# Optimization experiments

Hardware: AMD Instinct MI355X
Metric: run time of the kernel (lower is better)

Reference implementation:

```python
import jax, jax.numpy as jnp
import numpy as np

K = 64                      # sort-pool k
B_GRAPHS, N_PER = 256, 512  # graphs, nodes per graph
DIM_F, E_PER = 128, 8192    # node feature dim, edges per graph
EMB = 32


def setup_inputs() -> dict:
    key = jax.random.key(0)
    ks = jax.random.split(key, 12)
    N = B_GRAPHS * N_PER
    off = (jnp.arange(B_GRAPHS) * N_PER)[:, None]
    x = jax.random.normal(ks[0], (N, DIM_F), jnp.float32)
    edge_src = (jax.random.randint(ks[1], (B_GRAPHS, E_PER), 0, N_PER) + off).reshape(-1)
    edge_dst = (jax.random.randint(ks[2], (B_GRAPHS, E_PER), 0, N_PER) + off).reshape(-1)

    def lin(k, o, i):
        return (jax.random.normal(k, (o, i), jnp.float32) / np.float32(np.sqrt(i)))

    return {
        "x": x,
        "W0": lin(ks[3], EMB, DIM_F), "b0": jnp.zeros((EMB,), jnp.float32),
        "W1": lin(ks[4], EMB, EMB),   "b1": jnp.zeros((EMB,), jnp.float32),
        "W2": lin(ks[5], EMB, EMB),   "b2": jnp.zeros((EMB,), jnp.float32),
        "W3": lin(ks[6], 1, EMB),     "b3": jnp.zeros((1,), jnp.float32),
        "conv1_w": jax.random.normal(ks[7], (16, 1, 97), jnp.float32) / np.float32(np.sqrt(97.0)),
        "conv1_b": jnp.zeros((16,), jnp.float32),
        "conv2_w": jax.random.normal(ks[8], (32, 16, 5), jnp.float32) / np.float32(np.sqrt(80.0)),
        "conv2_b": jnp.zeros((32,), jnp.float32),
        "d1_w": lin(ks[9], 128, 896),  "d1_b": jnp.zeros((128,), jnp.float32),
        "d2_w": lin(ks[10], 10, 128),  "d2_b": jnp.zeros((10,), jnp.float32),
        "edge_src": edge_src, "edge_dst": edge_dst,
        "num_graphs": B_GRAPHS,
    }


def _dgcnn_conv(h_in, W, b, src, dst):
    # h = lin(x); message = (1/deg_src)[dst] * h[src]; scatter-add at dst
    N = h_in.shape[0]
    h = h_in @ W.T + b
    deg = jax.ops.segment_sum(jnp.ones_like(src, dtype=h.dtype), src, num_segments=N)
    norm = 1.0 / deg                       # self-loops guarantee deg >= 1
    msg = h[src] * norm[dst][:, None]      # [E+N, C]
    return jax.ops.segment_sum(msg, dst, num_segments=N)


def _forward(x, W0, b0, W1, b1, W2, b2, W3, b3,
             conv1_w, conv1_b, conv2_w, conv2_b,
             d1_w, d1_b, d2_w, d2_b, src, dst, num_graphs):
    N = x.shape[0]
    self_idx = jnp.arange(N)
    src = jnp.concatenate([src, self_idx])   # add_self_loops
    dst = jnp.concatenate([dst, self_idx])
    hs = []
    h = x
    for (W, b) in ((W0, b0), (W1, b1), (W2, b2), (W3, b3)):
        h = jnp.tanh(_dgcnn_conv(h, W, b, src, dst))
        hs.append(h)
    feat = jnp.concatenate(hs, axis=1)       # [N, 97]
    D = feat.shape[1]
    B = num_graphs
    n = N // B
    g = feat.reshape(B, n, D)
    # global_sort_pool: sort nodes per graph by last channel, descending, take top-k
    order = jnp.argsort(-g[:, :, -1], axis=1)[:, :K]
    topk = jnp.take_along_axis(g, order[:, :, None], axis=1)   # [B, K, D]
    # Conv1d(1,16,kernel=D,stride=D) over [B,1,K*D] == per-node linear on D
    c1 = jax.nn.relu(jnp.einsum('bkd,od->bok', topk, conv1_w[:, 0, :])
                     + conv1_b[None, :, None])                  # [B,16,K]
    p = c1.reshape(B, 16, K // 2, 2).max(axis=-1)               # MaxPool1d(2,2)
    c2 = jax.lax.conv_general_dilated(p, conv2_w, (1,), 'VALID',
                                      dimension_numbers=('NCH', 'OIH', 'NCH'))
    c2 = jax.nn.relu(c2 + conv2_b[None, :, None])               # [B,32,28]
    flat = c2.reshape(B, -1)                                    # [B,896]
    hid = jax.nn.relu(flat @ d1_w.T + d1_b)                     # dropout = identity (eval)
    return hid @ d2_w.T + d2_b                                  # [B,10]


def reference(x, W0, b0, W1, b1, W2, b2, W3, b3,
              conv1_w, conv1_b, conv2_w, conv2_b,
              d1_w, d1_b, d2_w, d2_b, edge_src, edge_dst, num_graphs):
    return _forward(x, W0, b0, W1, b1, W2, b2, W3, b3,
                    conv1_w, conv1_b, conv2_w, conv2_b,
                    d1_w, d1_b, d2_w, d2_b, edge_src, edge_dst, num_graphs)
```

## Files before the change

### kernel.cpp

```cpp
#include <hip/hip_runtime.h>

#define NG   256
#define NP   512
#define EPG  8192
#define FDIM 128
#define STB  36

#define OFF_STAGE 0
#define OFF_BUFB  65536
#define OFF_CSR   139264
#define OFF_OFFS  155648
#define OFF_WT    156680
#define OFF_CUR   156712
#define OFF_DCNT  158760
#define OFF_NRM   160808
#define SMEM_SZ   162856

#define OFF_KEY  OFF_CSR
#define OFF_IDX  (OFF_CSR + 2048)
#define OFF_L3   OFF_CUR
#define FO_FEAT 0
#define FO_C1   6208
#define FO_P    7232
#define FO_C2   7744
#define FO_HID  8640

__global__ __launch_bounds__(1024, 4) void dgcnn_fused(
    const float* __restrict__ x,
    const float* __restrict__ W0, const float* __restrict__ b0,
    const float* __restrict__ W1, const float* __restrict__ b1,
    const float* __restrict__ W2, const float* __restrict__ b2,
    const float* __restrict__ W3, const float* __restrict__ b3,
    const float* __restrict__ c1w, const float* __restrict__ c1b,
    const float* __restrict__ c2w, const float* __restrict__ c2b,
    const float* __restrict__ d1w, const float* __restrict__ d1b,
    const float* __restrict__ d2w, const float* __restrict__ d2b,
    const int* __restrict__ esrc, const int* __restrict__ edst,
    float* __restrict__ hs1, float* __restrict__ hs2,
    float* __restrict__ out)
{
  extern __shared__ char smem[];
  float*          stageF = (float*)(smem + OFF_STAGE);
  float*          bufB  = (float*)(smem + OFF_BUFB);
  unsigned short* csr   = (unsigned short*)(smem + OFF_CSR);
  unsigned short* offs  = (unsigned short*)(smem + OFF_OFFS);
  unsigned int*   wt    = (unsigned int*)(smem + OFF_WT);
  unsigned int*   cur   = (unsigned int*)(smem + OFF_CUR);
  unsigned int*   dcnt  = (unsigned int*)(smem + OFF_DCNT);
  float*          nrm   = (float*)(smem + OFF_NRM);
  float*          lin3S = (float*)(smem + OFF_L3);
  float*          keyA  = (float*)(smem + OFF_KEY);
  unsigned int*   idxA  = (unsigned int*)(smem + OFF_IDX);

  const int g    = blockIdx.x;
  const int tid  = threadIdx.x;
  const int lane = tid & 63;
  const int wv   = __builtin_amdgcn_readfirstlane(tid >> 6);
  const int half = __builtin_amdgcn_readfirstlane(tid >> 9);
  const int v    = tid & 511;
  const int nb   = g * NP;
  const size_t gb = (size_t)g * (NP * 32);

  const int ldRow0 = tid >> 3;
  const int ldGrp  = tid & 7;
  const int ldSwz  = (ldGrp ^ (ldRow0 & 7)) * 16;
  auto load_chunk = [&](int kc, float4* xr) {
    const float* base = x + (size_t)nb * FDIM + kc * 32 + ldGrp * 4;
#pragma unroll
    for (int it = 0; it < 4; it++)
      xr[it] = *(const float4*)(base + (size_t)(ldRow0 + it * 128) * FDIM);
  };
  auto store_chunk = [&](const float4* xr) {
#pragma unroll
    for (int it = 0; it < 4; it++)
      *(float4*)(smem + OFF_STAGE + (ldRow0 + it * 128) * 128 + ldSwz) = xr[it];
  };

  float4 xr[4], xr2[4];
  load_chunk(0, xr);

  if (tid < 512) { cur[tid] = 0u; dcnt[tid] = 0u; }
  __syncthreads();

  int es[8], ed[8];
  {
    const int eb = g * EPG;
    const int4* s4 = (const int4*)(esrc + eb);
    const int4* d4 = (const int4*)(edst + eb);
    const int4 sa = s4[tid], sb = s4[tid + 1024];
    const int4 da = d4[tid], db = d4[tid + 1024];
    es[0]=sa.x-nb; es[1]=sa.y-nb; es[2]=sa.z-nb; es[3]=sa.w-nb;
    es[4]=sb.x-nb; es[5]=sb.y-nb; es[6]=sb.z-nb; es[7]=sb.w-nb;
    ed[0]=da.x-nb; ed[1]=da.y-nb; ed[2]=da.z-nb; ed[3]=da.w-nb;
    ed[4]=db.x-nb; ed[5]=db.y-nb; ed[6]=db.z-nb; ed[7]=db.w-nb;
#pragma unroll
    for (int i = 0; i < 8; i++) {
      atomicAdd(&dcnt[es[i]], 1u);
      atomicAdd(&dcnt[ed[i]], 65536u);
    }
  }
  __syncthreads();

  unsigned c_scan = 0;
  if (tid < 512) {
    const unsigned cw = dcnt[tid];
    nrm[tid] = 1.0f / (float)((cw & 0xFFFFu) + 1u);
    c_scan = cw >> 16;
    for (int d = 1; d < 64; d <<= 1) {
      const unsigned t = __shfl_up(c_scan, (unsigned)d, 64);
      if (lane >= d) c_scan += t;
    }
    if (lane == 63) wt[wv] = c_scan;
  }
  __syncthreads();
  if (tid < 512) {
    unsigned base = 0;
    for (int w = 0; w < wv; w++) base += wt[w];
    offs[tid + 1] = (unsigned short)(base + c_scan);
    if (tid == 0) offs[0] = 0;
  }
  __syncthreads();

#pragma unroll
  for (int i = 0; i < 8; i++) {
    const unsigned pos = (unsigned)offs[ed[i]] + atomicAdd(&cur[ed[i]], 1u);
    csr[pos] = (unsigned short)es[i];
  }

  float acc0[16];
#pragma unroll
  for (int c = 0; c < 16; c++) acc0[c] = b0[half * 16 + c];
  const char* rowp = smem + OFF_STAGE + v * 128;
  const int vswz = v & 7;
  for (int kc = 0; kc < 4; kc++) {
    __syncthreads();
    store_chunk(xr);
    if (kc < 3) load_chunk(kc + 1, xr2);
    __syncthreads();
#pragma unroll
    for (int jg = 0; jg < 8; jg++) {
      const float4 t = *(const float4*)(rowp + ((jg ^ vswz) * 16));
#pragma unroll
      for (int c = 0; c < 16; c++) {
        const float* wr = W0 + (size_t)(half * 16 + c) * FDIM + kc * 32 + jg * 4;
        acc0[c] = fmaf(t.x, wr[0], acc0[c]);
        acc0[c] = fmaf(t.y, wr[1], acc0[c]);
        acc0[c] = fmaf(t.z, wr[2], acc0[c]);
        acc0[c] = fmaf(t.w, wr[3], acc0[c]);
      }
    }
#pragma unroll
    for (int it = 0; it < 4; it++) xr[it] = xr2[it];
  }
  {
    float4* br = (float4*)(bufB + v * STB + half * 16);
#pragma unroll
    for (int j = 0; j < 4; j++)
      br[j] = make_float4(acc0[j*4+0], acc0[j*4+1], acc0[j*4+2], acc0[j*4+3]);
  }
  __syncthreads();

  float h[16];
  auto do_agg = [&]() {
    float4 A0, A1, A2, A3;
    const float4* sr = (const float4*)(bufB + v * STB + half * 16);
    A0 = sr[0]; A1 = sr[1]; A2 = sr[2]; A3 = sr[3];
    const int e0 = offs[v], e1 = offs[v + 1];
    int e = e0;
    for (; e + 1 < e1; e += 2) {
      const int s0 = csr[e], s1 = csr[e + 1];
      const float4* rb0 = (const float4*)(bufB + s0 * STB + half * 16);
      const float4* rb1 = (const float4*)(bufB + s1 * STB + half * 16);
      const float4 p0 = rb0[0], p1 = rb0[1], p2 = rb0[2], p3 = rb0[3];
      const float4 q0 = rb1[0], q1 = rb1[1], q2 = rb1[2], q3 = rb1[3];
      A0.x += p0.x + q0.x; A0.y += p0.y + q0.y; A0.z += p0.z + q0.z; A0.w += p0.w + q0.w;
      A1.x += p1.x + q1.x; A1.y += p1.y + q1.y; A1.z += p1.z + q1.z; A1.w += p1.w + q1.w;
      A2.x += p2.x + q2.x; A2.y += p2.y + q2.y; A2.z += p2.z + q2.z; A2.w += p2.w + q2.w;
      A3.x += p3.x + q3.x; A3.y += p3.y + q3.y; A3.z += p3.z + q3.z; A3.w += p3.w + q3.w;
    }
    if (e < e1) {
      const int s = csr[e];
      const float4* rb = (const float4*)(bufB + s * STB + half * 16);
      const float4 r0 = rb[0], r1 = rb[1], r2 = rb[2], r3 = rb[3];
      A0.x += r0.x; A0.y += r0.y; A0.z += r0.z; A0.w += r0.w;
      A1.x += r1.x; A1.y += r1.y; A1.z += r1.z; A1.w += r1.w;
      A2.x += r2.x; A2.y += r2.y; A2.z += r2.z; A2.w += r2.w;
      A3.x += r3.x; A3.y += r3.y; A3.z += r3.z; A3.w += r3.w;
    }
    const float nv = nrm[v];
    h[0]=tanhf(A0.x*nv); h[1]=tanhf(A0.y*nv); h[2]=tanhf(A0.z*nv); h[3]=tanhf(A0.w*nv);
    h[4]=tanhf(A1.x*nv); h[5]=tanhf(A1.y*nv); h[6]=tanhf(A1.z*nv); h[7]=tanhf(A1.w*nv);
    h[8]=tanhf(A2.x*nv); h[9]=tanhf(A2.y*nv); h[10]=tanhf(A2.z*nv); h[11]=tanhf(A2.w*nv);
    h[12]=tanhf(A3.x*nv); h[13]=tanhf(A3.y*nv); h[14]=tanhf(A3.z*nv); h[15]=tanhf(A3.w*nv);
  };

  auto put_h = [&]() {
    float4* br = (float4*)(bufB + v * STB + half * 16);
#pragma unroll
    for (int j = 0; j < 4; j++)
      br[j] = make_float4(h[j*4+0], h[j*4+1], h[j*4+2], h[j*4+3]);
  };

  auto spill = [&](float* dst) {
#pragma unroll
    for (int c = 0; c < 16; c++)
      dst[gb + (size_t)(half * 16 + c) * 512 + v] = h[c];
  };

  auto do_lin = [&](const float* __restrict__ W, const float* __restrict__ b) {
    float hf[32];
    const float4* rr = (const float4*)(bufB + v * STB);
#pragma unroll
    for (int j = 0; j < 8; j++) {
      const float4 t = rr[j];
      hf[j*4+0]=t.x; hf[j*4+1]=t.y; hf[j*4+2]=t.z; hf[j*4+3]=t.w;
    }
    __syncthreads();
    float acc[16];
#pragma unroll
    for (int c = 0; c < 16; c++) {
      const int C = half * 16 + c;
      const float* wr = W + C * 32;
      float a = b[C];
#pragma unroll
      for (int j = 0; j < 32; j++) a = fmaf(hf[j], wr[j], a);
      acc[c] = a;
    }
    float4* br = (float4*)(bufB + v * STB + half * 16);
#pragma unroll
    for (int j = 0; j < 4; j++)
      br[j] = make_float4(acc[j*4+0], acc[j*4+1], acc[j*4+2], acc[j*4+3]);
    __syncthreads();
  };

  do_agg();
  __syncthreads();
  put_h(); spill(hs1);
  __syncthreads();
  do_lin(W1, b1);
  do_agg();
  __syncthreads();
  put_h(); spill(hs2);
  __syncthreads();
  do_lin(W2, b2);
  do_agg();
  __syncthreads();
  put_h();
  __syncthreads();

  if (tid < 512) {
    const float4* rr = (const float4*)(bufB + tid * STB);
    double a = (double)b3[0];
#pragma unroll
    for (int j = 0; j < 8; j++) {
      const float4 t = rr[j];
      a = fma((double)t.x, (double)W3[j*4+0], a);
      a = fma((double)t.y, (double)W3[j*4+1], a);
      a = fma((double)t.z, (double)W3[j*4+2], a);
      a = fma((double)t.w, (double)W3[j*4+3], a);
    }
    lin3S[tid] = (float)a;
  }
  __syncthreads();
  float h4 = 0.f;
  if (tid < 512) {
    double a = (double)lin3S[tid];
    const int e0 = offs[tid], e1 = offs[tid + 1];
    for (int e = e0; e < e1; e++) a += (double)lin3S[csr[e]];
    a *= (double)nrm[tid];
    h4 = tanhf((float)a);
  }
  __syncthreads();
  if (tid < 512) { keyA[tid] = h4; idxA[tid] = (unsigned)tid; }

  for (int k = 2; k <= NP; k <<= 1) {
    for (int j = k >> 1; j > 0; j >>= 1) {
      __syncthreads();
      if (tid < 512) {
        const int i = tid;
        const int l = i ^ j;
        if (l > i) {
          const float    ki = keyA[i], kl = keyA[l];
          const unsigned ii = idxA[i], il = idxA[l];
          const bool iBeforeL = (ki > kl) || (ki == kl && ii < il);
          const bool doSwap = ((i & k) == 0) ? (!iBeforeL) : iBeforeL;
          if (doSwap) {
            keyA[i] = kl; keyA[l] = ki;
            idxA[i] = il; idxA[l] = ii;
          }
        }
      }
    }
  }
  __syncthreads();

  {
    float* featS = stageF + FO_FEAT;
    const int k = tid >> 4, t = tid & 15;
    const int node = (int)idxA[k];
#pragma unroll
    for (int m = 0; m < 7; m++) {
      const int d = t + 16 * m;
      float val;
      if (d < 32)       val = hs1[gb + (size_t)d * 512 + node];
      else if (d < 64)  val = hs2[gb + (size_t)(d - 32) * 512 + node];
      else if (d < 96)  val = bufB[node * STB + (d - 64)];
      else              val = keyA[k];
      if (d < 97) featS[d * 64 + k] = val;
    }
  }
  __syncthreads();

  {
    const float* featS = stageF + FO_FEAT;
    float* c1s = stageF + FO_C1;
    const int ch = wv;
    double a = (double)c1b[ch];
    const float* wr = c1w + ch * 97;
    for (int d = 0; d < 97; d++)
      a = fma((double)featS[d * 64 + lane], (double)wr[d], a);
    c1s[ch * 64 + lane] = fmaxf((float)a, 0.f);
  }
  __syncthreads();

  if (tid < 512) {
    const float* c1s = stageF + FO_C1;
    float* ps  = stageF + FO_P;
    const int o = tid >> 5, jj = tid & 31;
    ps[o * 32 + jj] = fmaxf(c1s[o * 64 + 2 * jj], c1s[o * 64 + 2 * jj + 1]);
  }
  __syncthreads();

  {
    const float* ps  = stageF + FO_P;
    float* c2s = stageF + FO_C2;
    const int o = wv;
    if (lane < 28) {
      double a0 = 0., a1 = 0.;
      for (int i = 0; i < 16; i++) {
#pragma unroll
        for (int r = 0; r < 5; r++) {
          const double pv = (double)ps[i * 32 + lane + r];
          a0 = fma(pv, (double)c2w[((o     ) * 16 + i) * 5 + r], a0);
          a1 = fma(pv, (double)c2w[((o + 16) * 16 + i) * 5 + r], a1);
        }
      }
      c2s[(o     ) * 28 + lane] = fmaxf((float)(a0 + (double)c2b[o     ]), 0.f);
      c2s[(o + 16) * 28 + lane] = fmaxf((float)(a1 + (double)c2b[o + 16]), 0.f);
    }
  }
  __syncthreads();

  {
    const float* c2s  = stageF + FO_C2;
    float* hids = stageF + FO_HID;
    float fl[14];
#pragma unroll
    for (int j = 0; j < 14; j++) fl[j] = c2s[lane + j * 64];
    for (int hh = 0; hh < 8; hh++) {
      const int hI = wv * 8 + hh;
      const float* wr = d1w + (size_t)hI * 896;
      double a = 0.;
#pragma unroll
      for (int j = 0; j < 14; j++) a = fma((double)fl[j], (double)wr[lane + j * 64], a);
#pragma unroll
      for (int m = 32; m > 0; m >>= 1) a += __shfl_xor(a, m, 64);
      if (lane == 0) hids[hI] = fmaxf((float)(a + (double)d1b[hI]), 0.f);
    }
  }
  __syncthreads();

  if (tid < 10) {
    const float* hids = stageF + FO_HID;
    const float* wr = d2w + tid * 128;
    double a = (double)d2b[tid];
#pragma unroll 8
    for (int hh = 0; hh < 128; hh++) a = fma((double)hids[hh], (double)wr[hh], a);
    out[g * 10 + tid] = (float)a;
  }
}

extern "C" void kernel_launch(void* const* d_in, const int* in_sizes, int n_in,
                              void* d_out, int out_size, void* d_ws, size_t ws_size,
                              hipStream_t stream) {
  const float* x   = (const float*)d_in[0];
  const float* W0  = (const float*)d_in[1];
  const float* b0  = (const float*)d_in[2];
  const float* W1  = (const float*)d_in[3];
  const float* b1  = (const float*)d_in[4];
  const float* W2  = (const float*)d_in[5];
  const float* b2  = (const float*)d_in[6];
  const float* W3  = (const float*)d_in[7];
  const float* b3  = (const float*)d_in[8];
  const float* c1w = (const float*)d_in[9];
  const float* c1b = (const float*)d_in[10];
  const float* c2w = (const float*)d_in[11];
  const float* c2b = (const float*)d_in[12];
  const float* d1w = (const float*)d_in[13];
  const float* d1b = (const float*)d_in[14];
  const float* d2w = (const float*)d_in[15];
  const float* d2b = (const float*)d_in[16];
  const int* esrc  = (const int*)d_in[17];
  const int* edst  = (const int*)d_in[18];

  float* hs1 = (float*)d_ws;
  float* hs2 = hs1 + (size_t)NG * NP * 32;
  float* outp = (float*)d_out;

  hipFuncSetAttribute(reinterpret_cast<const void*>(dgcnn_fused),
                      hipFuncAttributeMaxDynamicSharedMemorySize, SMEM_SZ);
  dgcnn_fused<<<NG, 1024, SMEM_SZ, stream>>>(x, W0, b0, W1, b1, W2, b2, W3, b3,
                                             c1w, c1b, c2w, c2b, d1w, d1b, d2w, d2b,
                                             esrc, edst, hs1, hs2, outp);
}
```

Before: 279.5 us.

## Use fp32 in head layers, warp-shuffle bitonic stages, unroll feature-load loop

The conv1, conv2 and two dense head layers now accumulate in fp32 fmaf instead of fp64 fma, which removes slow double-precision arithmetic. The first bitonic sort stages (up to size 64) now run inside a wavefront with shuffles, which removes many __syncthreads and shared-memory round trips. The first-layer chunk loop is manually unrolled with ping-pong register buffers so the copy between buffers disappears. Switching to fp32 changes rounding in the head and could affect tolerance.

```diff
diff --git a/kernel.cpp b/kernel.cpp
--- a/kernel.cpp
+++ b/kernel.cpp
@@ -76,8 +76,8 @@
       *(float4*)(smem + OFF_STAGE + (ldRow0 + it * 128) * 128 + ldSwz) = xr[it];
   };
 
-  float4 xr[4], xr2[4];
-  load_chunk(0, xr);
+  float4 xa[4], xb[4];
+  load_chunk(0, xa);
 
   if (tid < 512) { cur[tid] = 0u; dcnt[tid] = 0u; }
   __syncthreads();
@@ -132,11 +132,7 @@
   for (int c = 0; c < 16; c++) acc0[c] = b0[half * 16 + c];
   const char* rowp = smem + OFF_STAGE + v * 128;
   const int vswz = v & 7;
-  for (int kc = 0; kc < 4; kc++) {
-    __syncthreads();
-    store_chunk(xr);
-    if (kc < 3) load_chunk(kc + 1, xr2);
-    __syncthreads();
+  auto compute_chunk = [&](int kc) {
 #pragma unroll
     for (int jg = 0; jg < 8; jg++) {
       const float4 t = *(const float4*)(rowp + ((jg ^ vswz) * 16));
@@ -149,9 +145,25 @@
         acc0[c] = fmaf(t.w, wr[3], acc0[c]);
       }
     }
-#pragma unroll
-    for (int it = 0; it < 4; it++) xr[it] = xr2[it];
-  }
+  };
+  store_chunk(xa);
+  __syncthreads();
+  load_chunk(1, xb);
+  compute_chunk(0);
+  __syncthreads();
+  store_chunk(xb);
+  __syncthreads();
+  load_chunk(2, xa);
+  compute_chunk(1);
+  __syncthreads();
+  store_chunk(xa);
+  __syncthreads();
+  load_chunk(3, xb);
+  compute_chunk(2);
+  __syncthreads();
+  store_chunk(xb);
+  __syncthreads();
+  compute_chunk(3);
   {
     float4* br = (float4*)(bufB + v * STB + half * 16);
 #pragma unroll
@@ -271,9 +283,27 @@
     h4 = tanhf((float)a);
   }
   __syncthreads();
-  if (tid < 512) { keyA[tid] = h4; idxA[tid] = (unsigned)tid; }
-
-  for (int k = 2; k <= NP; k <<= 1) {
+
+  if (tid < 512) {
+    float    sk = h4;
+    unsigned si = (unsigned)tid;
+#pragma unroll
+    for (int kk = 2; kk <= 64; kk <<= 1) {
+#pragma unroll
+      for (int j = kk >> 1; j > 0; j >>= 1) {
+        const float    pk = __shfl_xor(sk, j, 64);
+        const unsigned pi = __shfl_xor(si, j, 64);
+        const bool amFirst = (sk > pk) || (sk == pk && si < pi);
+        const bool lower   = (lane & j) == 0;
+        const bool dir     = (tid & kk) == 0;
+        const bool keepMine = (lower == dir) ? amFirst : !amFirst;
+        if (!keepMine) { sk = pk; si = pi; }
+      }
+    }
+    keyA[tid] = sk;
+    idxA[tid] = si;
+  }
+  for (int k = 128; k <= NP; k <<= 1) {
     for (int j = k >> 1; j > 0; j >>= 1) {
       __syncthreads();
       if (tid < 512) {
@@ -315,11 +345,11 @@
     const float* featS = stageF + FO_FEAT;
     float* c1s = stageF + FO_C1;
     const int ch = wv;
-    double a = (double)c1b[ch];
+    float a = c1b[ch];
     const float* wr = c1w + ch * 97;
     for (int d = 0; d < 97; d++)
-      a = fma((double)featS[d * 64 + lane], (double)wr[d], a);
-    c1s[ch * 64 + lane] = fmaxf((float)a, 0.f);
+      a = fmaf(featS[d * 64 + lane], wr[d], a);
+    c1s[ch * 64 + lane] = fmaxf(a, 0.f);
   }
   __syncthreads();
 
@@ -336,17 +366,17 @@
     float* c2s = stageF + FO_C2;
     const int o = wv;
     if (lane < 28) {
-      double a0 = 0., a1 = 0.;
+      float a0 = 0.f, a1 = 0.f;
       for (int i = 0; i < 16; i++) {
 #pragma unroll
         for (int r = 0; r < 5; r++) {
-          const double pv = (double)ps[i * 32 + lane + r];
-          a0 = fma(pv, (double)c2w[((o     ) * 16 + i) * 5 + r], a0);
-          a1 = fma(pv, (double)c2w[((o + 16) * 16 + i) * 5 + r], a1);
+          const float pv = ps[i * 32 + lane + r];
+          a0 = fmaf(pv, c2w[((o     ) * 16 + i) * 5 + r], a0);
+          a1 = fmaf(pv, c2w[((o + 16) * 16 + i) * 5 + r], a1);
         }
       }
-      c2s[(o     ) * 28 + lane] = fmaxf((float)(a0 + (double)c2b[o     ]), 0.f);
-      c2s[(o + 16) * 28 + lane] = fmaxf((float)(a1 + (double)c2b[o + 16]), 0.f);
+      c2s[(o     ) * 28 + lane] = fmaxf(a0 + c2b[o     ], 0.f);
+      c2s[(o + 16) * 28 + lane] = fmaxf(a1 + c2b[o + 16], 0.f);
     }
   }
   __syncthreads();
@@ -360,12 +390,12 @@
     for (int hh = 0; hh < 8; hh++) {
       const int hI = wv * 8 + hh;
       const float* wr = d1w + (size_t)hI * 896;
-      double a = 0.;
-#pragma unroll
-      for (int j = 0; j < 14; j++) a = fma((double)fl[j], (double)wr[lane + j * 64], a);
+      float a = 0.f;
+#pragma unroll
+      for (int j = 0; j < 14; j++) a = fmaf(fl[j], wr[lane + j * 64], a);
 #pragma unroll
       for (int m = 32; m > 0; m >>= 1) a += __shfl_xor(a, m, 64);
-      if (lane == 0) hids[hI] = fmaxf((float)(a + (double)d1b[hI]), 0.f);
+      if (lane == 0) hids[hI] = fmaxf(a + d1b[hI], 0.f);
     }
   }
   __syncthreads();
@@ -373,10 +403,10 @@
   if (tid < 10) {
     const float* hids = stageF + FO_HID;
     const float* wr = d2w + tid * 128;
-    double a = (double)d2b[tid];
+    float a = d2b[tid];
 #pragma unroll 8
-    for (int hh = 0; hh < 128; hh++) a = fma((double)hids[hh], (double)wr[hh], a);
-    out[g * 10 + tid] = (float)a;
+    for (int hh = 0; hh < 128; hh++) a = fmaf(hids[hh], wr[hh], a);
+    out[g * 10 + tid] = a;
   }
 }
 
```

Measured after the change: 505.9 us. +81.0%, slower.
